# Kernel tuning notes

Measured on AMD Instinct MI355X. Metric: run time of the kernel, lower is better.

Reference implementation:

```python
import jax, jax.numpy as jnp
import numpy as np

NUM_EMBEDDINGS = 8192
EMBEDDING_DIM = 256


def setup_inputs() -> dict:
    key = jax.random.key(0)
    k1, k2 = jax.random.split(key)
    z = jax.random.normal(k1, (16, EMBEDDING_DIM, 32, 32), dtype=jnp.float32)
    # nn.Embedding default init: N(0, 1)
    emb_table = jax.random.normal(k2, (NUM_EMBEDDINGS, EMBEDDING_DIM), dtype=jnp.float32)
    return {"z": z, "emb_table": emb_table}


def reference(z, emb_table):
    # z: [B, D, H, W]; emb_table: [K, D]
    B, D, H, W = z.shape
    # flatten to per-token vectors: [B*H*W, D]
    zf = z.reshape(B, D, H * W).transpose(0, 2, 1).reshape(B * H * W, D)
    Wt = jax.lax.stop_gradient(emb_table)  # original detaches W for distance
    # argmin of mean squared distance == argmin of squared distance;
    # expand ||z - w||^2 = ||z||^2 - 2 z.w + ||w||^2 (avoid (N,K,D) expansion)
    z_sq = jnp.sum(zf * zf, axis=-1, keepdims=True)          # [N, 1]
    w_sq = jnp.sum(Wt * Wt, axis=-1)                          # [K]
    dists = z_sq - 2.0 * (zf @ Wt.T) + w_sq                   # [N, K]
    token_ids = jnp.argmin(dists, axis=-1)                    # [N]
    quantized = emb_table[token_ids]                          # [N, D] (differentiable gather)
    return quantized.reshape(B, H * W, D).transpose(0, 2, 1).reshape(B, D, H, W)
```

## Files before the change

kernel.cpp:

```cpp
#include <hip/hip_runtime.h>
#include <stdint.h>

#define DIM 256
#define NEMB 8192
#define NTOK 16384
#define HW 1024

typedef __attribute__((ext_vector_type(4))) int int4v;

__device__ __forceinline__ void async_cp16(void* lds, const void* g) {
  __builtin_amdgcn_global_load_lds(
      (const __attribute__((address_space(1))) unsigned int*)g,
      (__attribute__((address_space(3))) unsigned int*)lds, 16, 0, 0);
}
__device__ __forceinline__ int q0_of(float x) {
  int q = __float2int_rn(x * 20.0f);
  return q > 127 ? 127 : (q < -127 ? -127 : q);
}
__device__ __forceinline__ int q1_of(float x, int q0) {
  float e = x * 20.0f - (float)q0;
  int q = __float2int_rn(e * 128.0f);
  return q > 127 ? 127 : (q < -127 ? -127 : q);
}
__device__ __forceinline__ unsigned int pack4(int a, int b, int c, int d) {
  return (unsigned int)(a & 0xff) | ((unsigned int)(b & 0xff) << 8) |
         ((unsigned int)(c & 0xff) << 16) | ((unsigned int)(d & 0xff) << 24);
}
__device__ __forceinline__ unsigned int med3u(unsigned int a, unsigned int b,
                                              unsigned int c) {
  unsigned int m;
  asm("v_med3_u32 %0, %1, %2, %3" : "=v"(m) : "v"(a), "v"(b), "v"(c));
  return m;
}
__device__ __forceinline__ void top3_insert(unsigned int v, unsigned int& m1,
                                            unsigned int& m2, unsigned int& m3) {
  unsigned int t2 = med3u(v, m1, m2);
  unsigned int t3 = med3u(v, m2, m3);
  m1 = v < m1 ? v : m1;
  m2 = t2;
  m3 = t3;
}

__global__ __launch_bounds__(256) void prep_kernel(
    const float* __restrict__ emb, unsigned int* __restrict__ q0w,
    unsigned int* __restrict__ q1w, int* __restrict__ iwsq2,
    const float* __restrict__ z, unsigned int* __restrict__ q0z) {
  __shared__ float tile[64][65];
  int tid = threadIdx.x;
  int lane = tid & 63;
  if (blockIdx.x < 2048) {
    int row = blockIdx.x * 4 + (tid >> 6);
    const float4 v = *(const float4*)(emb + (size_t)row * DIM + lane * 4);
    float s = v.x * v.x + v.y * v.y + v.z * v.z + v.w * v.w;
    int a0 = q0_of(v.x), b0 = q0_of(v.y), c0 = q0_of(v.z), d0 = q0_of(v.w);
    q0w[row * (DIM / 4) + lane] = pack4(a0, b0, c0, d0);
    q1w[row * (DIM / 4) + lane] =
        pack4(q1_of(v.x, a0), q1_of(v.y, b0), q1_of(v.z, c0), q1_of(v.w, d0));
#pragma unroll
    for (int off = 32; off > 0; off >>= 1) s += __shfl_xor(s, off, 64);
    if (lane == 0) iwsq2[row] = (int)rintf(s * 25600.0f) + 8192;
    return;
  }
  int idx = blockIdx.x - 2048;
  int b = idx >> 6, d0 = ((idx >> 4) & 3) * 64, hw0 = (idx & 15) * 64;
  int grp = tid >> 6;
  const float* src = z + (size_t)b * DIM * HW + hw0 + lane;
#pragma unroll
  for (int i = 0; i < 16; i++) {
    int dl = grp + i * 4;
    tile[dl][lane] = src[(size_t)(d0 + dl) * HW];
  }
  __syncthreads();
  int dq = tid & 15;
#pragma unroll
  for (int p = 0; p < 4; p++) {
    int n = (tid >> 4) + p * 16;
    int a0 = q0_of(tile[dq * 4 + 0][n]), b0 = q0_of(tile[dq * 4 + 1][n]);
    int c0 = q0_of(tile[dq * 4 + 2][n]), e0 = q0_of(tile[dq * 4 + 3][n]);
    int token = b * HW + hw0 + n;
    q0z[(size_t)token * (DIM / 4) + (d0 >> 2) + dq] = pack4(a0, b0, c0, e0);
  }
}

__global__ __launch_bounds__(256, 4) void gemm_topk_kernel(
    const signed char* __restrict__ q0z, const signed char* __restrict__ q0w,
    const signed char* __restrict__ q1w, const int* __restrict__ iwsq2,
    uint4* __restrict__ partials) {
  __shared__ __align__(16) signed char sB[2][4][32 * 128];

  const int bid = blockIdx.x;
  const int kq = bid & 7;
  const int tg = bid >> 3;
  const int tid = threadIdx.x;
  const int lane = tid & 63, w = tid >> 6;
  const int c = lane & 15, quad = lane >> 4;
  const int n0 = tg * 128;
  const int k0g = kq * 1024;

  int4v af0[2][4];
#pragma unroll
  for (int t = 0; t < 2; t++) {
    const size_t arow = (size_t)(n0 + w * 32 + t * 16 + c) * DIM;
#pragma unroll
    for (int s = 0; s < 4; s++)
      af0[t][s] = *(const int4v*)(q0z + arow + s * 64 + quad * 16);
  }

  const int srow = tid >> 3;
  const int scl = ((tid & 7) ^ (srow & 7)) * 16;
  const signed char* p0 = q0w + (size_t)(k0g + srow) * DIM + scl;
  const signed char* p1 = q1w + (size_t)(k0g + srow) * DIM + scl;
  async_cp16(&sB[0][0][tid * 16], p0);
  async_cp16(&sB[0][1][tid * 16], p0 + 128);
  async_cp16(&sB[0][2][tid * 16], p1);
  async_cp16(&sB[0][3][tid * 16], p1 + 128);
  p0 += 32 * DIM;
  p1 += 32 * DIM;
  __syncthreads();

  unsigned int m1[8], m2[8], m3[8];
#pragma unroll
  for (int i = 0; i < 8; i++) {
    m1[i] = 0xFFFFFFFFu; m2[i] = 0xFFFFFFFFu; m3[i] = 0xFFFFFFFFu;
  }

  unsigned int idxA = (unsigned)(k0g + c);
  const int4v zero = {0, 0, 0, 0};

  for (int it = 0; it < 32; it++) {
    const int buf = it & 1;
    if (it + 1 < 32) {
      const int nb = buf ^ 1;
      async_cp16(&sB[nb][0][tid * 16], p0);
      async_cp16(&sB[nb][1][tid * 16], p0 + 128);
      async_cp16(&sB[nb][2][tid * 16], p1);
      async_cp16(&sB[nb][3][tid * 16], p1 + 128);
      p0 += 32 * DIM;
      p1 += 32 * DIM;
    }
    const int iw0 = iwsq2[k0g + it * 32 + c];
    const int iw1 = iwsq2[k0g + it * 32 + 16 + c];

    int4v a[2][2];
#pragma unroll
    for (int s = 0; s < 4; s++) {
      const int ph = ((((s & 1) << 2) + quad) ^ (c & 7)) * 16;
      int4v b0a = *(const int4v*)(&sB[buf][s >> 1][c * 128 + ph]);
      int4v b0b = *(const int4v*)(&sB[buf][s >> 1][(16 + c) * 128 + ph]);
      if (s == 0) {
#pragma unroll
        for (int t = 0; t < 2; t++) {
          a[t][0] = __builtin_amdgcn_mfma_i32_16x16x64_i8(af0[t][0], b0a, zero, 0, 0, 0);
          a[t][1] = __builtin_amdgcn_mfma_i32_16x16x64_i8(af0[t][0], b0b, zero, 0, 0, 0);
        }
      } else {
#pragma unroll
        for (int t = 0; t < 2; t++) {
          a[t][0] = __builtin_amdgcn_mfma_i32_16x16x64_i8(af0[t][s], b0a, a[t][0], 0, 0, 0);
          a[t][1] = __builtin_amdgcn_mfma_i32_16x16x64_i8(af0[t][s], b0b, a[t][1], 0, 0, 0);
        }
      }
    }
#pragma unroll
    for (int t = 0; t < 2; t++)
#pragma unroll
      for (int cn = 0; cn < 2; cn++)
#pragma unroll
        for (int r = 0; r < 4; r++) a[t][cn][r] <<= 7;
#pragma unroll
    for (int s = 0; s < 4; s++) {
      const int ph = ((((s & 1) << 2) + quad) ^ (c & 7)) * 16;
      int4v b1a = *(const int4v*)(&sB[buf][2 + (s >> 1)][c * 128 + ph]);
      int4v b1b = *(const int4v*)(&sB[buf][2 + (s >> 1)][(16 + c) * 128 + ph]);
#pragma unroll
      for (int t = 0; t < 2; t++) {
        a[t][0] = __builtin_amdgcn_mfma_i32_16x16x64_i8(af0[t][s], b1a, a[t][0], 0, 0, 0);
        a[t][1] = __builtin_amdgcn_mfma_i32_16x16x64_i8(af0[t][s], b1b, a[t][1], 0, 0, 0);
      }
    }
#pragma unroll
    for (int t = 0; t < 2; t++) {
#pragma unroll
      for (int r = 0; r < 4; r++) {
        unsigned int s0 = (unsigned int)(iw0 - a[t][0][r]);
        unsigned int s1 = (unsigned int)(iw1 - a[t][1][r]);
        s0 = s0 < 0x2000000u ? s0 : 0x1FFFFFFu;
        s1 = s1 < 0x2000000u ? s1 : 0x1FFFFFFu;
        unsigned int pk0 = ((s0 << 7) & 0xFFFFE000u) | idxA;
        unsigned int pk1 = ((s1 << 7) & 0xFFFFE000u) | (idxA + 16);
        top3_insert(pk0 < pk1 ? pk0 : pk1, m1[t * 4 + r], m2[t * 4 + r],
                    m3[t * 4 + r]);
      }
    }
    idxA += 32;
    __syncthreads();
  }

#pragma unroll
  for (int ix = 0; ix < 8; ix++) {
    unsigned int a1 = m1[ix], a2 = m2[ix], a3 = m3[ix];
#pragma unroll
    for (int off = 1; off < 16; off <<= 1) {
      unsigned int o1 = __shfl_xor(a1, off, 16);
      unsigned int o2 = __shfl_xor(a2, off, 16);
      unsigned int o3 = __shfl_xor(a3, off, 16);
      top3_insert(o1, a1, a2, a3);
      top3_insert(o2, a1, a2, a3);
      top3_insert(o3, a1, a2, a3);
    }
    m1[ix] = a1; m2[ix] = a2; m3[ix] = a3;
  }
  if (c == 0) {
#pragma unroll
    for (int t = 0; t < 2; t++) {
#pragma unroll
      for (int r = 0; r < 4; r++) {
        int token = n0 + w * 32 + t * 16 + quad * 4 + r;
        partials[(size_t)kq * NTOK + token] =
            make_uint4(m1[t * 4 + r], m2[t * 4 + r], m3[t * 4 + r], 0xFFFFFFFFu);
      }
    }
  }
}

__global__ __launch_bounds__(256) void rescore_gather_kernel(
    const uint4* __restrict__ partials, const float* __restrict__ z,
    const float* __restrict__ emb, float* __restrict__ out) {
  __shared__ float tile[32][257];
  __shared__ int sid[32];
  __shared__ int wl[32];
  __shared__ int nwl;
  const int b = blockIdx.x >> 5;
  const int hw0 = (blockIdx.x & 31) * 32;
  const int tid = threadIdx.x;
  if (tid == 0) nwl = 0;
  __syncthreads();
  {
    const int tl = tid >> 3, sub = tid & 7;
    const int token = b * HW + hw0 + tl;
    uint4 e = partials[(size_t)sub * NTOK + token];
    unsigned int m = e.x < e.y ? e.x : e.y;
    m = e.z < m ? e.z : m;
#pragma unroll
    for (int off = 1; off < 8; off <<= 1) {
      unsigned int o = __shfl_xor(m, off, 8);
      m = o < m ? o : m;
    }
    const unsigned int thr = (m >> 13) + 1536;
    int cnt = (((e.x >> 13) <= thr) ? 1 : 0) + (((e.y >> 13) <= thr) ? 1 : 0) +
              (((e.z >> 13) <= thr) ? 1 : 0);
#pragma unroll
    for (int off = 1; off < 8; off <<= 1) cnt += __shfl_xor(cnt, off, 8);
    if (sub == 0) {
      if (cnt == 1) {
        sid[tl] = (int)(m & 0x1FFFu);
      } else {
        int i = atomicAdd(&nwl, 1);
        wl[i] = tl;
      }
    }
  }
  __syncthreads();
  {
    const int w = tid >> 6, lane = tid & 63;
    for (int i = w; i < nwl; i += 4) {
      const int tl = wl[i];
      const int token = b * HW + hw0 + tl;
      unsigned int p[24];
#pragma unroll
      for (int q = 0; q < 8; q++) {
        uint4 t = partials[(size_t)q * NTOK + token];
        p[q * 3] = t.x;
        p[q * 3 + 1] = t.y;
        p[q * 3 + 2] = t.z;
      }
      unsigned int smin = p[0];
#pragma unroll
      for (int q = 1; q < 24; q++) smin = p[q] < smin ? p[q] : smin;
      const unsigned int thr = (smin >> 13) + 1536;
      float zv[4];
#pragma unroll
      for (int j = 0; j < 4; j++)
        zv[j] = z[(size_t)b * DIM * HW + (size_t)(lane * 4 + j) * HW + hw0 + tl];
      double best = 1e300;
      int bid2 = NEMB;
#pragma unroll
      for (int q = 0; q < 24; q++) {
        if ((p[q] >> 13) <= thr) {
          int id = (int)(p[q] & 0x1FFFu);
          const float4 wv = *(const float4*)(emb + (size_t)id * DIM + lane * 4);
          double s = (double)wv.x * ((double)wv.x - 2.0 * (double)zv[0]) +
                     (double)wv.y * ((double)wv.y - 2.0 * (double)zv[1]) +
                     (double)wv.z * ((double)wv.z - 2.0 * (double)zv[2]) +
                     (double)wv.w * ((double)wv.w - 2.0 * (double)zv[3]);
#pragma unroll
          for (int off = 32; off > 0; off >>= 1) s += __shfl_xor(s, off, 64);
          if (s < best || (s == best && id < bid2)) {
            best = s;
            bid2 = id;
          }
        }
      }
      if (lane == 0) sid[tl] = bid2;
    }
  }
  __syncthreads();
  for (int i = 0; i < 32; i++)
    tile[i][tid] = emb[(size_t)sid[i] * DIM + tid];
  __syncthreads();
  int h = tid & 31, dg = tid >> 5;
  for (int i = 0; i < 32; i++) {
    int d = i * 8 + dg;
    out[(size_t)b * DIM * HW + (size_t)d * HW + hw0 + h] = tile[h][d];
  }
}

extern "C" void kernel_launch(void* const* d_in, const int* in_sizes, int n_in,
                              void* d_out, int out_size, void* d_ws, size_t ws_size,
                              hipStream_t stream) {
  const float* z = (const float*)d_in[0];
  const float* emb = (const float*)d_in[1];
  float* out = (float*)d_out;
  char* ws = (char*)d_ws;

  signed char* q0w = (signed char*)(ws);
  signed char* q1w = (signed char*)(ws + 2097152);
  signed char* q0z = (signed char*)(ws + 4194304);
  int* iwsq2 = (int*)(ws + 8388608);
  uint4* partials = (uint4*)(ws + 8421376);

  prep_kernel<<<dim3(3072), 256, 0, stream>>>(
      emb, (unsigned int*)q0w, (unsigned int*)q1w, iwsq2, z, (unsigned int*)q0z);
  gemm_topk_kernel<<<dim3(1024), 256, 0, stream>>>(q0z, q0w, q1w, iwsq2,
                                                   partials);
  rescore_gather_kernel<<<dim3(512), 256, 0, stream>>>(partials, z, emb, out);
}
```

Measured before the change: 169.9 us.

## Double GEMM block to 512 threads sharing codebook tiles; simplify top-k key packing

The GEMM/top-k kernel now runs 512 threads per block over 256 tokens instead of 256 threads over 128, so each codebook tile staged in LDS is reused by twice as many waves and the grid is halved. The async copy is split so half the threads load q0w and half load q1w, two copies each. The score packing first takes the min of the two candidate scores, then clamps, shifts and packs once, instead of packing both and comparing. Larger blocks cut global traffic for the codebook but drop the occupancy hint and may change register pressure and scheduling.

```diff
diff --git a/kernel.cpp b/kernel.cpp
--- a/kernel.cpp
+++ b/kernel.cpp
@@ -82,7 +82,7 @@
   }
 }
 
-__global__ __launch_bounds__(256, 4) void gemm_topk_kernel(
+__global__ __launch_bounds__(512) void gemm_topk_kernel(
     const signed char* __restrict__ q0z, const signed char* __restrict__ q0w,
     const signed char* __restrict__ q1w, const int* __restrict__ iwsq2,
     uint4* __restrict__ partials) {
@@ -94,7 +94,7 @@
   const int tid = threadIdx.x;
   const int lane = tid & 63, w = tid >> 6;
   const int c = lane & 15, quad = lane >> 4;
-  const int n0 = tg * 128;
+  const int n0 = tg * 256;
   const int k0g = kq * 1024;
 
   int4v af0[2][4];
@@ -106,16 +106,16 @@
       af0[t][s] = *(const int4v*)(q0z + arow + s * 64 + quad * 16);
   }
 
-  const int srow = tid >> 3;
-  const int scl = ((tid & 7) ^ (srow & 7)) * 16;
-  const signed char* p0 = q0w + (size_t)(k0g + srow) * DIM + scl;
-  const signed char* p1 = q1w + (size_t)(k0g + srow) * DIM + scl;
-  async_cp16(&sB[0][0][tid * 16], p0);
-  async_cp16(&sB[0][1][tid * 16], p0 + 128);
-  async_cp16(&sB[0][2][tid * 16], p1);
-  async_cp16(&sB[0][3][tid * 16], p1 + 128);
-  p0 += 32 * DIM;
-  p1 += 32 * DIM;
+  const int hi = tid >> 8;
+  const int t2 = tid & 255;
+  const int srow = t2 >> 3;
+  const int scl = ((t2 & 7) ^ (srow & 7)) * 16;
+  const signed char* p = (hi ? q1w : q0w) + (size_t)(k0g + srow) * DIM + scl;
+  signed char* d0s = &sB[0][hi * 2][t2 * 16];
+  signed char* d1s = &sB[0][hi * 2 + 1][t2 * 16];
+  async_cp16(d0s, p);
+  async_cp16(d1s, p + 128);
+  p += 32 * DIM;
   __syncthreads();
 
   unsigned int m1[8], m2[8], m3[8];
@@ -131,12 +131,9 @@
     const int buf = it & 1;
     if (it + 1 < 32) {
       const int nb = buf ^ 1;
-      async_cp16(&sB[nb][0][tid * 16], p0);
-      async_cp16(&sB[nb][1][tid * 16], p0 + 128);
-      async_cp16(&sB[nb][2][tid * 16], p1);
-      async_cp16(&sB[nb][3][tid * 16], p1 + 128);
-      p0 += 32 * DIM;
-      p1 += 32 * DIM;
+      async_cp16(d0s + nb * 16384, p);
+      async_cp16(d1s + nb * 16384, p + 128);
+      p += 32 * DIM;
     }
     const int iw0 = iwsq2[k0g + it * 32 + c];
     const int iw1 = iwsq2[k0g + it * 32 + 16 + c];
@@ -184,12 +181,11 @@
       for (int r = 0; r < 4; r++) {
         unsigned int s0 = (unsigned int)(iw0 - a[t][0][r]);
         unsigned int s1 = (unsigned int)(iw1 - a[t][1][r]);
-        s0 = s0 < 0x2000000u ? s0 : 0x1FFFFFFu;
-        s1 = s1 < 0x2000000u ? s1 : 0x1FFFFFFu;
-        unsigned int pk0 = ((s0 << 7) & 0xFFFFE000u) | idxA;
-        unsigned int pk1 = ((s1 << 7) & 0xFFFFE000u) | (idxA + 16);
-        top3_insert(pk0 < pk1 ? pk0 : pk1, m1[t * 4 + r], m2[t * 4 + r],
-                    m3[t * 4 + r]);
+        unsigned int smin = s0 < s1 ? s0 : s1;
+        unsigned int idx = s1 < s0 ? idxA + 16 : idxA;
+        smin = smin < 0x1FFFFFFu ? smin : 0x1FFFFFFu;
+        unsigned int pk = ((smin >> 6) << 13) | idx;
+        top3_insert(pk, m1[t * 4 + r], m2[t * 4 + r], m3[t * 4 + r]);
       }
     }
     idxA += 32;
@@ -331,7 +327,7 @@
 
   prep_kernel<<<dim3(3072), 256, 0, stream>>>(
       emb, (unsigned int*)q0w, (unsigned int*)q1w, iwsq2, z, (unsigned int*)q0z);
-  gemm_topk_kernel<<<dim3(1024), 256, 0, stream>>>(q0z, q0w, q1w, iwsq2,
-                                                   partials);
+  gemm_topk_kernel<<<dim3(512), 512, 0, stream>>>(q0z, q0w, q1w, iwsq2,
+                                                  partials);
   rescore_gather_kernel<<<dim3(512), 256, 0, stream>>>(partials, z, emb, out);
 }
```

Result: faster. 159.7 us (-6.0%).
